# Optimization experiments

Hardware: AMD Instinct MI355X
Metric: run time of the kernel (lower is better)

The kernel has to match this reference:

```python
import jax, jax.numpy as jnp
import numpy as np

K, Q, DIM = 64, 128, 1024
TF_W, DE_W, FFT_W = 1.0, 0.8, 0.6  # opt.TF_weight / DE_weight / FFT_weight


def setup_inputs() -> dict:
    key = jax.random.key(0)
    ks = jax.random.split(key, 9)
    def feats(k):
        return jax.random.normal(k, (K, Q, DIM), dtype=jnp.float32)
    def protos(k):
        return jax.random.normal(k, (K, DIM), dtype=jnp.float32)
    def var(k):
        # positive variances, bounded away from zero
        return jax.random.uniform(k, (K,), dtype=jnp.float32) + 0.5
    return {
        "TFq_output": feats(ks[0]), "TFs_proto": protos(ks[1]), "TF_variance": var(ks[2]),
        "DEq_output": feats(ks[3]), "DEs_proto": protos(ks[4]), "DE_variance": var(ks[5]),
        "FFTq_output": feats(ks[6]), "FFTs_proto": protos(ks[7]), "FFT_variance": var(ks[8]),
    }


def _mah_dist(xq, proto, variance):
    # ||x - p||^2 / var via expansion: avoids materializing (num, protonum, dim)
    x2 = jnp.sum(xq * xq, axis=1, keepdims=True)            # (num, 1)
    p2 = jnp.sum(proto * proto, axis=1)[None, :]            # (1, protonum)
    xp = xq @ proto.T                                       # (num, protonum)
    return (x2 - 2.0 * xp + p2) / variance[None, :]


def _modality(xq, proto, variance, w):
    logits = -_mah_dist(xq, proto, variance)
    pred = w * jax.nn.softmax(logits, axis=1)
    mahloss = -(w * jax.nn.log_softmax(logits, axis=1))
    return pred, mahloss


def reference(TFq_output, TFs_proto, TF_variance,
              DEq_output, DEs_proto, DE_variance,
              FFTq_output, FFTs_proto, FFT_variance):
    k, q, _ = TFq_output.shape
    y = jnp.repeat(jnp.arange(k), q)                         # (k*q,)

    tf_pred, tf_loss = _modality(TFq_output.reshape(k * q, -1), TFs_proto, TF_variance, TF_W)
    de_pred, de_loss = _modality(DEq_output.reshape(k * q, -1), DEs_proto, DE_variance, DE_W)
    fft_pred, fft_loss = _modality(FFTq_output.reshape(k * q, -1), FFTs_proto, FFT_variance, FFT_W)

    fusion_loss = tf_loss + de_loss + fft_loss               # (k*q, k)
    loss = jnp.take_along_axis(fusion_loss, y[:, None], axis=1).squeeze(-1).mean()

    pred_mah = tf_pred + de_pred + fft_pred
    pred = jnp.argmax(pred_mah, axis=1)
    acc = (pred == y).astype(jnp.float32).mean()
    return (loss, acc)
```

## Files before the change

kernel.cpp:

```cpp
#include <hip/hip_runtime.h>


typedef _Float16 half8 __attribute__((ext_vector_type(8)));
typedef float    floatx4 __attribute__((ext_vector_type(4)));

#define NCLS   64
#define QPC    128
#define DIM    1024
#define NROWS  (NCLS * QPC)
#define KSPLIT 4
#define KSLICE (DIM / KSPLIT)
#define NITER  (KSLICE / 32)
#define NWAVES 12
#define DSTRIDE 17
#define PSTRIDE 65

#define WPROTO_BYTES (3 * NCLS * DIM * 2)
#define WS_NEED      (WPROTO_BYTES + 3 * NCLS * 4)

__global__ __launch_bounds__(64) void prep_protos(
    const float* __restrict__ Ptf, const float* __restrict__ Pde,
    const float* __restrict__ Pff, _Float16* __restrict__ W,
    float* __restrict__ p2)
{
    const int m    = blockIdx.x >> 5;
    const int kcg  = blockIdx.x & 31;
    const int lane = threadIdx.x;
    const int l15  = lane & 15;
    const int quad = lane >> 4;
    const float* __restrict__ P = (m == 0) ? Ptf : (m == 1) ? Pde : Pff;

    #pragma unroll
    for (int t = 0; t < 4; ++t) {
        const float* src = P + (size_t)(t * 16 + l15) * DIM + kcg * 32 + quad * 8;
        const float4 b0 = *reinterpret_cast<const float4*>(src);
        const float4 b1 = *reinterpret_cast<const float4*>(src + 4);
        half8 h;
        h[0] = (_Float16)b0.x; h[1] = (_Float16)b0.y;
        h[2] = (_Float16)b0.z; h[3] = (_Float16)b0.w;
        h[4] = (_Float16)b1.x; h[5] = (_Float16)b1.y;
        h[6] = (_Float16)b1.z; h[7] = (_Float16)b1.w;
        *reinterpret_cast<half8*>(W + ((size_t)(m * 32 + kcg) * 4 + t) * 512 + lane * 8) = h;

        float s = b0.x*b0.x + b0.y*b0.y + b0.z*b0.z + b0.w*b0.w
                + b1.x*b1.x + b1.y*b1.y + b1.z*b1.z + b1.w*b1.w;
        s += __shfl_xor(s, 16);
        s += __shfl_xor(s, 32);
        if (quad == 0) atomicAdd(&p2[m * 64 + t * 16 + l15], s);
    }
}

__global__ __launch_bounds__(NWAVES * 64, 3) void fusion_loss_kernel(
    const float* __restrict__ Xtf, const float* __restrict__ Vtf,
    const float* __restrict__ Xde, const float* __restrict__ Vde,
    const float* __restrict__ Xff, const float* __restrict__ Vff,
    const _Float16* __restrict__ W, const float* __restrict__ p2g,
    float* __restrict__ out)
{
    __shared__ float dpart[NWAVES][64 * DSTRIDE];
    __shared__ float x2part[NWAVES][16];
    __shared__ float predL[16 * PSTRIDE];
    __shared__ float lossL;

    const int tid  = threadIdx.x;
    const int wave = tid >> 6;
    const int lane = tid & 63;
    const int l15  = lane & 15;
    const int quad = lane >> 4;
    const int m    = wave >> 2;
    const int kq   = wave & 3;
    const int rowBase = blockIdx.x * 16;

    for (int i = tid; i < 16 * PSTRIDE; i += NWAVES * 64) predL[i] = 0.0f;
    if (tid == 0) lossL = 0.0f;

    const float* __restrict__ X = (m == 0) ? Xtf : (m == 1) ? Xde : Xff;
    const float* __restrict__ V = (m == 0) ? Vtf : (m == 1) ? Vde : Vff;
    const float  w = (m == 0) ? 1.0f : (m == 1) ? 0.8f : 0.6f;

    floatx4 d[4];
    #pragma unroll
    for (int t = 0; t < 4; ++t) d[t] = (floatx4){0.f, 0.f, 0.f, 0.f};
    float x2p = 0.0f;

    const float* xrow = X + (size_t)(rowBase + l15) * DIM + kq * KSLICE + quad * 8;
    const _Float16* wbase = W + (size_t)(m * 32 + kq * NITER) * 4 * 512 + lane * 8;

    #pragma unroll 4
    for (int kc = 0; kc < NITER; ++kc) {
        const int ko = kc * 32;
        const float4 a0 = *reinterpret_cast<const float4*>(xrow + ko);
        const float4 a1 = *reinterpret_cast<const float4*>(xrow + ko + 4);
        half8 bf[4];
        #pragma unroll
        for (int t = 0; t < 4; ++t)
            bf[t] = *reinterpret_cast<const half8*>(wbase + (size_t)(kc * 4 + t) * 512);

        x2p += a0.x*a0.x + a0.y*a0.y + a0.z*a0.z + a0.w*a0.w
             + a1.x*a1.x + a1.y*a1.y + a1.z*a1.z + a1.w*a1.w;

        half8 af;
        af[0] = (_Float16)a0.x; af[1] = (_Float16)a0.y;
        af[2] = (_Float16)a0.z; af[3] = (_Float16)a0.w;
        af[4] = (_Float16)a1.x; af[5] = (_Float16)a1.y;
        af[6] = (_Float16)a1.z; af[7] = (_Float16)a1.w;

        #pragma unroll
        for (int t = 0; t < 4; ++t)
            d[t] = __builtin_amdgcn_mfma_f32_16x16x32_f16(af, bf[t], d[t], 0, 0, 0);
    }

    x2p += __shfl_xor(x2p, 16);
    x2p += __shfl_xor(x2p, 32);

    {
        float* dp = &dpart[wave][lane * DSTRIDE];
        #pragma unroll
        for (int t = 0; t < 4; ++t)
            *reinterpret_cast<float4*>(dp + t * 4) =
                make_float4(d[t][0], d[t][1], d[t][2], d[t][3]);
        if (quad == 0) x2part[wave][l15] = x2p;
    }
    __syncthreads();

    const int y = rowBase >> 7;

    if (kq == 0) {
        floatx4 dsum[4];
        #pragma unroll
        for (int t = 0; t < 4; ++t) dsum[t] = (floatx4){0.f, 0.f, 0.f, 0.f};
        float x2r[4] = {0.f, 0.f, 0.f, 0.f};
        #pragma unroll
        for (int k2 = 0; k2 < KSPLIT; ++k2) {
            const int wv = m * 4 + k2;
            const float* src = &dpart[wv][lane * DSTRIDE];
            #pragma unroll
            for (int t = 0; t < 4; ++t) {
                const float4 v = *reinterpret_cast<const float4*>(src + t * 4);
                dsum[t][0] += v.x; dsum[t][1] += v.y; dsum[t][2] += v.z; dsum[t][3] += v.w;
            }
            #pragma unroll
            for (int r = 0; r < 4; ++r) x2r[r] += x2part[wv][quad * 4 + r];
        }
        float vc[4], p2c[4];
        #pragma unroll
        for (int t = 0; t < 4; ++t) {
            vc[t]  = V[t * 16 + l15];
            p2c[t] = p2g[m * 64 + t * 16 + l15];
        }

        float lossAcc = 0.0f;
        #pragma unroll
        for (int r = 0; r < 4; ++r) {
            float lg[4];
            #pragma unroll
            for (int t = 0; t < 4; ++t)
                lg[t] = (2.0f * dsum[t][r] - x2r[r] - p2c[t]) / vc[t];

            float mx = fmaxf(fmaxf(lg[0], lg[1]), fmaxf(lg[2], lg[3]));
            #pragma unroll
            for (int dl = 1; dl <= 8; dl <<= 1) mx = fmaxf(mx, __shfl_xor(mx, dl));
            float s = expf(lg[0] - mx) + expf(lg[1] - mx)
                    + expf(lg[2] - mx) + expf(lg[3] - mx);
            #pragma unroll
            for (int dl = 1; dl <= 8; dl <<= 1) s += __shfl_xor(s, dl);
            const float lse = mx + logf(s);

            const int row = quad * 4 + r;
            #pragma unroll
            for (int t = 0; t < 4; ++t) {
                const int col = t * 16 + l15;
                if (col == y) lossAcc += w * (lse - lg[t]);
                atomicAdd(&predL[row * PSTRIDE + col], w * expf(lg[t] - lse));
            }
        }
        #pragma unroll
        for (int dl = 1; dl <= 32; dl <<= 1) lossAcc += __shfl_xor(lossAcc, dl);
        if (lane == 0) atomicAdd(&lossL, lossAcc);
    }
    __syncthreads();

    if (wave == 0) {
        float cnt = 0.0f;
        #pragma unroll 1
        for (int r = 0; r < 16; ++r) {
            float bv = predL[r * PSTRIDE + lane];
            int   bc = lane;
            #pragma unroll
            for (int dl = 1; dl <= 32; dl <<= 1) {
                const float ov = __shfl_xor(bv, dl);
                const int   oc = __shfl_xor(bc, dl);
                if (ov > bv || (ov == bv && oc < bc)) { bv = ov; bc = oc; }
            }
            if (lane == 0 && bc == y) cnt += 1.0f;
        }
        if (lane == 0) {
            atomicAdd(&out[0], lossL * (1.0f / NROWS));
            atomicAdd(&out[1], cnt * (1.0f / NROWS));
        }
    }
}

__global__ __launch_bounds__(NWAVES * 64) void fusion_loss_fallback(
    const float* __restrict__ Xtf, const float* __restrict__ Ptf, const float* __restrict__ Vtf,
    const float* __restrict__ Xde, const float* __restrict__ Pde, const float* __restrict__ Vde,
    const float* __restrict__ Xff, const float* __restrict__ Pff, const float* __restrict__ Vff,
    float* __restrict__ out)
{
    __shared__ float dpart[NWAVES][64 * DSTRIDE];
    __shared__ float x2part[NWAVES][16];
    __shared__ float p2part[NWAVES][64];
    __shared__ float predL[16 * PSTRIDE];
    __shared__ float lossL;

    const int tid  = threadIdx.x;
    const int wave = tid >> 6;
    const int lane = tid & 63;
    const int l15  = lane & 15;
    const int quad = lane >> 4;
    const int m    = wave >> 2;
    const int kq   = wave & 3;
    const int rowBase = blockIdx.x * 16;

    for (int i = tid; i < 16 * PSTRIDE; i += NWAVES * 64) predL[i] = 0.0f;
    if (tid == 0) lossL = 0.0f;

    const float* __restrict__ X = (m == 0) ? Xtf : (m == 1) ? Xde : Xff;
    const float* __restrict__ P = (m == 0) ? Ptf : (m == 1) ? Pde : Pff;
    const float* __restrict__ V = (m == 0) ? Vtf : (m == 1) ? Vde : Vff;
    const float  w = (m == 0) ? 1.0f : (m == 1) ? 0.8f : 0.6f;

    floatx4 d[4];
    #pragma unroll
    for (int t = 0; t < 4; ++t) d[t] = (floatx4){0.f, 0.f, 0.f, 0.f};
    float x2p    = 0.0f;
    float p2p[4] = {0.f, 0.f, 0.f, 0.f};

    const float* xrow = X + (size_t)(rowBase + l15) * DIM + kq * KSLICE + quad * 8;
    const float* prow[4];
    #pragma unroll
    for (int t = 0; t < 4; ++t)
        prow[t] = P + (size_t)(t * 16 + l15) * DIM + kq * KSLICE + quad * 8;

    #pragma unroll 2
    for (int kc = 0; kc < NITER; ++kc) {
        const int ko = kc * 32;
        const float4 a0 = *reinterpret_cast<const float4*>(xrow + ko);
        const float4 a1 = *reinterpret_cast<const float4*>(xrow + ko + 4);
        float4 b0[4], b1[4];
        #pragma unroll
        for (int t = 0; t < 4; ++t) {
            b0[t] = *reinterpret_cast<const float4*>(prow[t] + ko);
            b1[t] = *reinterpret_cast<const float4*>(prow[t] + ko + 4);
        }
        x2p += a0.x*a0.x + a0.y*a0.y + a0.z*a0.z + a0.w*a0.w
             + a1.x*a1.x + a1.y*a1.y + a1.z*a1.z + a1.w*a1.w;
        half8 af;
        af[0] = (_Float16)a0.x; af[1] = (_Float16)a0.y;
        af[2] = (_Float16)a0.z; af[3] = (_Float16)a0.w;
        af[4] = (_Float16)a1.x; af[5] = (_Float16)a1.y;
        af[6] = (_Float16)a1.z; af[7] = (_Float16)a1.w;
        #pragma unroll
        for (int t = 0; t < 4; ++t) {
            p2p[t] += b0[t].x*b0[t].x + b0[t].y*b0[t].y + b0[t].z*b0[t].z + b0[t].w*b0[t].w
                    + b1[t].x*b1[t].x + b1[t].y*b1[t].y + b1[t].z*b1[t].z + b1[t].w*b1[t].w;
            half8 bf;
            bf[0] = (_Float16)b0[t].x; bf[1] = (_Float16)b0[t].y;
            bf[2] = (_Float16)b0[t].z; bf[3] = (_Float16)b0[t].w;
            bf[4] = (_Float16)b1[t].x; bf[5] = (_Float16)b1[t].y;
            bf[6] = (_Float16)b1[t].z; bf[7] = (_Float16)b1[t].w;
            d[t] = __builtin_amdgcn_mfma_f32_16x16x32_f16(af, bf, d[t], 0, 0, 0);
        }
    }

    x2p += __shfl_xor(x2p, 16);
    x2p += __shfl_xor(x2p, 32);
    #pragma unroll
    for (int t = 0; t < 4; ++t) {
        p2p[t] += __shfl_xor(p2p[t], 16);
        p2p[t] += __shfl_xor(p2p[t], 32);
    }
    {
        float* dp = &dpart[wave][lane * DSTRIDE];
        #pragma unroll
        for (int t = 0; t < 4; ++t)
            *reinterpret_cast<float4*>(dp + t * 4) =
                make_float4(d[t][0], d[t][1], d[t][2], d[t][3]);
        if (quad == 0) {
            x2part[wave][l15] = x2p;
            #pragma unroll
            for (int t = 0; t < 4; ++t) p2part[wave][t * 16 + l15] = p2p[t];
        }
    }
    __syncthreads();

    const int y = rowBase >> 7;

    if (kq == 0) {
        floatx4 dsum[4];
        #pragma unroll
        for (int t = 0; t < 4; ++t) dsum[t] = (floatx4){0.f, 0.f, 0.f, 0.f};
        float x2r[4] = {0.f, 0.f, 0.f, 0.f};
        float p2c[4] = {0.f, 0.f, 0.f, 0.f};
        #pragma unroll
        for (int k2 = 0; k2 < KSPLIT; ++k2) {
            const int wv = m * 4 + k2;
            const float* src = &dpart[wv][lane * DSTRIDE];
            #pragma unroll
            for (int t = 0; t < 4; ++t) {
                const float4 v = *reinterpret_cast<const float4*>(src + t * 4);
                dsum[t][0] += v.x; dsum[t][1] += v.y; dsum[t][2] += v.z; dsum[t][3] += v.w;
            }
            #pragma unroll
            for (int r = 0; r < 4; ++r) x2r[r] += x2part[wv][quad * 4 + r];
            #pragma unroll
            for (int t = 0; t < 4; ++t) p2c[t] += p2part[wv][t * 16 + l15];
        }
        float vc[4];
        #pragma unroll
        for (int t = 0; t < 4; ++t) vc[t] = V[t * 16 + l15];

        float lossAcc = 0.0f;
        #pragma unroll
        for (int r = 0; r < 4; ++r) {
            float lg[4];
            #pragma unroll
            for (int t = 0; t < 4; ++t)
                lg[t] = (2.0f * dsum[t][r] - x2r[r] - p2c[t]) / vc[t];
            float mx = fmaxf(fmaxf(lg[0], lg[1]), fmaxf(lg[2], lg[3]));
            #pragma unroll
            for (int dl = 1; dl <= 8; dl <<= 1) mx = fmaxf(mx, __shfl_xor(mx, dl));
            float s = expf(lg[0] - mx) + expf(lg[1] - mx)
                    + expf(lg[2] - mx) + expf(lg[3] - mx);
            #pragma unroll
            for (int dl = 1; dl <= 8; dl <<= 1) s += __shfl_xor(s, dl);
            const float lse = mx + logf(s);
            const int row = quad * 4 + r;
            #pragma unroll
            for (int t = 0; t < 4; ++t) {
                const int col = t * 16 + l15;
                if (col == y) lossAcc += w * (lse - lg[t]);
                atomicAdd(&predL[row * PSTRIDE + col], w * expf(lg[t] - lse));
            }
        }
        #pragma unroll
        for (int dl = 1; dl <= 32; dl <<= 1) lossAcc += __shfl_xor(lossAcc, dl);
        if (lane == 0) atomicAdd(&lossL, lossAcc);
    }
    __syncthreads();

    if (wave == 0) {
        float cnt = 0.0f;
        #pragma unroll 1
        for (int r = 0; r < 16; ++r) {
            float bv = predL[r * PSTRIDE + lane];
            int   bc = lane;
            #pragma unroll
            for (int dl = 1; dl <= 32; dl <<= 1) {
                const float ov = __shfl_xor(bv, dl);
                const int   oc = __shfl_xor(bc, dl);
                if (ov > bv || (ov == bv && oc < bc)) { bv = ov; bc = oc; }
            }
            if (lane == 0 && bc == y) cnt += 1.0f;
        }
        if (lane == 0) {
            atomicAdd(&out[0], lossL * (1.0f / NROWS));
            atomicAdd(&out[1], cnt * (1.0f / NROWS));
        }
    }
}

extern "C" void kernel_launch(void* const* d_in, const int* in_sizes, int n_in,
                              void* d_out, int out_size, void* d_ws, size_t ws_size,
                              hipStream_t stream) {
    const float* Xtf = (const float*)d_in[0];
    const float* Ptf = (const float*)d_in[1];
    const float* Vtf = (const float*)d_in[2];
    const float* Xde = (const float*)d_in[3];
    const float* Pde = (const float*)d_in[4];
    const float* Vde = (const float*)d_in[5];
    const float* Xff = (const float*)d_in[6];
    const float* Pff = (const float*)d_in[7];
    const float* Vff = (const float*)d_in[8];
    float* out = (float*)d_out;

    hipMemsetAsync(out, 0, 2 * sizeof(float), stream);

    if (ws_size >= (size_t)WS_NEED) {
        _Float16* W  = (_Float16*)d_ws;
        float*    p2 = (float*)((char*)d_ws + WPROTO_BYTES);
        hipMemsetAsync(p2, 0, 3 * NCLS * sizeof(float), stream);
        prep_protos<<<dim3(96), dim3(64), 0, stream>>>(Ptf, Pde, Pff, W, p2);
        fusion_loss_kernel<<<dim3(NROWS / 16), dim3(NWAVES * 64), 0, stream>>>(
            Xtf, Vtf, Xde, Vde, Xff, Vff, W, p2, out);
    } else {
        fusion_loss_fallback<<<dim3(NROWS / 16), dim3(NWAVES * 64), 0, stream>>>(
            Xtf, Ptf, Vtf, Xde, Pde, Vde, Xff, Pff, Vff, out);
    }
}
```

Baseline: 170.3 us.

## Split modalities across blocks, stage X via LDS DMA, finalize with separate kernels

```diff
diff --git a/kernel.cpp b/kernel.cpp
--- a/kernel.cpp
+++ b/kernel.cpp
@@ -8,15 +8,27 @@
 #define QPC    128
 #define DIM    1024
 #define NROWS  (NCLS * QPC)
-#define KSPLIT 4
-#define KSLICE (DIM / KSPLIT)
-#define NITER  (KSLICE / 32)
-#define NWAVES 12
-#define DSTRIDE 17
-#define PSTRIDE 65
-
-#define WPROTO_BYTES (3 * NCLS * DIM * 2)
-#define WS_NEED      (WPROTO_BYTES + 3 * NCLS * 4)
+#define NRT    (NROWS / 16)
+#define CHUNK  256
+#define NCHUNK (DIM / CHUNK)
+#define NKC    (CHUNK / 32)
+#define UW     264
+
+#define OFF_W    0
+#define W_BYTES  (3 * NCLS * DIM * 2)
+#define OFF_P2   W_BYTES
+#define OFF_PRED 397312
+#define PRED_BYTES (3 * NROWS * NCLS * 4)
+#define OFF_LOSS (OFF_PRED + PRED_BYTES)
+#define OFF_CNT  (OFF_LOSS + 1536 * 4)
+#define WS_NEED  (OFF_CNT + 64 * 4)
+
+__device__ __forceinline__ void dma16(const float* g, float* l) {
+    __builtin_amdgcn_global_load_lds(
+        (const __attribute__((address_space(1))) void*)g,
+        (__attribute__((address_space(3))) void*)l,
+        16, 0, 0);
+}
 
 __global__ __launch_bounds__(64) void prep_protos(
     const float* __restrict__ Ptf, const float* __restrict__ Pde,
@@ -50,156 +62,197 @@
     }
 }
 
-__global__ __launch_bounds__(NWAVES * 64, 3) void fusion_loss_kernel(
+__global__ __launch_bounds__(128) void fusion_main(
     const float* __restrict__ Xtf, const float* __restrict__ Vtf,
     const float* __restrict__ Xde, const float* __restrict__ Vde,
     const float* __restrict__ Xff, const float* __restrict__ Vff,
     const _Float16* __restrict__ W, const float* __restrict__ p2g,
-    float* __restrict__ out)
+    float* __restrict__ predOut,
+    float* __restrict__ lossPart)
 {
-    __shared__ float dpart[NWAVES][64 * DSTRIDE];
-    __shared__ float x2part[NWAVES][16];
-    __shared__ float predL[16 * PSTRIDE];
-    __shared__ float lossL;
+    __shared__ float chunkBuf[16 * UW];
+    __shared__ float mxW[2][16], sW[2][16];
+    __shared__ float lossW[2];
 
     const int tid  = threadIdx.x;
-    const int wave = tid >> 6;
+    const int w    = tid >> 6;
     const int lane = tid & 63;
     const int l15  = lane & 15;
     const int quad = lane >> 4;
-    const int m    = wave >> 2;
-    const int kq   = wave & 3;
-    const int rowBase = blockIdx.x * 16;
-
-    for (int i = tid; i < 16 * PSTRIDE; i += NWAVES * 64) predL[i] = 0.0f;
-    if (tid == 0) lossL = 0.0f;
+    const int m    = blockIdx.x >> 9;
+    const int rt   = blockIdx.x & 511;
+    const int rowBase = rt * 16;
 
     const float* __restrict__ X = (m == 0) ? Xtf : (m == 1) ? Xde : Xff;
     const float* __restrict__ V = (m == 0) ? Vtf : (m == 1) ? Vde : Vff;
-    const float  w = (m == 0) ? 1.0f : (m == 1) ? 0.8f : 0.6f;
-
-    floatx4 d[4];
-    #pragma unroll
-    for (int t = 0; t < 4; ++t) d[t] = (floatx4){0.f, 0.f, 0.f, 0.f};
+    const float  wgt = (m == 0) ? 1.0f : (m == 1) ? 0.8f : 0.6f;
+
+    floatx4 d[2];
+    d[0] = (floatx4){0.f, 0.f, 0.f, 0.f};
+    d[1] = (floatx4){0.f, 0.f, 0.f, 0.f};
     float x2p = 0.0f;
 
-    const float* xrow = X + (size_t)(rowBase + l15) * DIM + kq * KSLICE + quad * 8;
-    const _Float16* wbase = W + (size_t)(m * 32 + kq * NITER) * 4 * 512 + lane * 8;
-
-    #pragma unroll 4
-    for (int kc = 0; kc < NITER; ++kc) {
-        const int ko = kc * 32;
-        const float4 a0 = *reinterpret_cast<const float4*>(xrow + ko);
-        const float4 a1 = *reinterpret_cast<const float4*>(xrow + ko + 4);
-        half8 bf[4];
-        #pragma unroll
-        for (int t = 0; t < 4; ++t)
-            bf[t] = *reinterpret_cast<const half8*>(wbase + (size_t)(kc * 4 + t) * 512);
-
-        x2p += a0.x*a0.x + a0.y*a0.y + a0.z*a0.z + a0.w*a0.w
-             + a1.x*a1.x + a1.y*a1.y + a1.z*a1.z + a1.w*a1.w;
-
-        half8 af;
-        af[0] = (_Float16)a0.x; af[1] = (_Float16)a0.y;
-        af[2] = (_Float16)a0.z; af[3] = (_Float16)a0.w;
-        af[4] = (_Float16)a1.x; af[5] = (_Float16)a1.y;
-        af[6] = (_Float16)a1.z; af[7] = (_Float16)a1.w;
-
-        #pragma unroll
-        for (int t = 0; t < 4; ++t)
-            d[t] = __builtin_amdgcn_mfma_f32_16x16x32_f16(af, bf[t], d[t], 0, 0, 0);
+    #pragma unroll 1
+    for (int c = 0; c < NCHUNK; ++c) {
+        __syncthreads();
+        const float* gbase = X + (size_t)rowBase * DIM + c * CHUNK + lane * 4;
+        #pragma unroll
+        for (int r8 = 0; r8 < 8; ++r8) {
+            const int r = w * 8 + r8;
+            dma16(gbase + (size_t)r * DIM, &chunkBuf[r * UW]);
+        }
+        __syncthreads();
+
+        #pragma unroll
+        for (int kc = 0; kc < NKC; ++kc) {
+            const int off = l15 * UW + kc * 32 + quad * 8;
+            const float4 a0 = *reinterpret_cast<const float4*>(&chunkBuf[off]);
+            const float4 a1 = *reinterpret_cast<const float4*>(&chunkBuf[off + 4]);
+
+            const int kcg = c * NKC + kc;
+            half8 bf[2];
+            #pragma unroll
+            for (int t = 0; t < 2; ++t)
+                bf[t] = *reinterpret_cast<const half8*>(
+                    W + ((size_t)(m * 32 + kcg) * 4 + (w * 2 + t)) * 512 + lane * 8);
+
+            x2p += a0.x*a0.x + a0.y*a0.y + a0.z*a0.z + a0.w*a0.w
+                 + a1.x*a1.x + a1.y*a1.y + a1.z*a1.z + a1.w*a1.w;
+
+            half8 af;
+            af[0] = (_Float16)a0.x; af[1] = (_Float16)a0.y;
+            af[2] = (_Float16)a0.z; af[3] = (_Float16)a0.w;
+            af[4] = (_Float16)a1.x; af[5] = (_Float16)a1.y;
+            af[6] = (_Float16)a1.z; af[7] = (_Float16)a1.w;
+
+            d[0] = __builtin_amdgcn_mfma_f32_16x16x32_f16(af, bf[0], d[0], 0, 0, 0);
+            d[1] = __builtin_amdgcn_mfma_f32_16x16x32_f16(af, bf[1], d[1], 0, 0, 0);
+        }
     }
 
     x2p += __shfl_xor(x2p, 16);
     x2p += __shfl_xor(x2p, 32);
-
-    {
-        float* dp = &dpart[wave][lane * DSTRIDE];
-        #pragma unroll
-        for (int t = 0; t < 4; ++t)
-            *reinterpret_cast<float4*>(dp + t * 4) =
-                make_float4(d[t][0], d[t][1], d[t][2], d[t][3]);
-        if (quad == 0) x2part[wave][l15] = x2p;
+    float x2r[4];
+    #pragma unroll
+    for (int r = 0; r < 4; ++r) x2r[r] = __shfl(x2p, quad * 4 + r);
+
+    float vc[2], p2c[2];
+    #pragma unroll
+    for (int t = 0; t < 2; ++t) {
+        const int col = w * 32 + t * 16 + l15;
+        vc[t]  = V[col];
+        p2c[t] = p2g[m * 64 + col];
+    }
+
+    float lg[4][2];
+    #pragma unroll
+    for (int r = 0; r < 4; ++r)
+        #pragma unroll
+        for (int t = 0; t < 2; ++t)
+            lg[r][t] = (2.0f * d[t][r] - x2r[r] - p2c[t]) / vc[t];
+
+    #pragma unroll
+    for (int r = 0; r < 4; ++r) {
+        float mx = fmaxf(lg[r][0], lg[r][1]);
+        #pragma unroll
+        for (int dl = 1; dl <= 8; dl <<= 1) mx = fmaxf(mx, __shfl_xor(mx, dl));
+        if (l15 == 0) mxW[w][quad * 4 + r] = mx;
+    }
+    __syncthreads();
+    float gmx[4];
+    #pragma unroll
+    for (int r = 0; r < 4; ++r) {
+        const int row = quad * 4 + r;
+        gmx[r] = fmaxf(mxW[0][row], mxW[1][row]);
+        float s = expf(lg[r][0] - gmx[r]) + expf(lg[r][1] - gmx[r]);
+        #pragma unroll
+        for (int dl = 1; dl <= 8; dl <<= 1) s += __shfl_xor(s, dl);
+        if (l15 == 0) sW[w][row] = s;
     }
     __syncthreads();
 
     const int y = rowBase >> 7;
-
-    if (kq == 0) {
-        floatx4 dsum[4];
-        #pragma unroll
-        for (int t = 0; t < 4; ++t) dsum[t] = (floatx4){0.f, 0.f, 0.f, 0.f};
-        float x2r[4] = {0.f, 0.f, 0.f, 0.f};
-        #pragma unroll
-        for (int k2 = 0; k2 < KSPLIT; ++k2) {
-            const int wv = m * 4 + k2;
-            const float* src = &dpart[wv][lane * DSTRIDE];
-            #pragma unroll
-            for (int t = 0; t < 4; ++t) {
-                const float4 v = *reinterpret_cast<const float4*>(src + t * 4);
-                dsum[t][0] += v.x; dsum[t][1] += v.y; dsum[t][2] += v.z; dsum[t][3] += v.w;
-            }
-            #pragma unroll
-            for (int r = 0; r < 4; ++r) x2r[r] += x2part[wv][quad * 4 + r];
-        }
-        float vc[4], p2c[4];
-        #pragma unroll
-        for (int t = 0; t < 4; ++t) {
-            vc[t]  = V[t * 16 + l15];
-            p2c[t] = p2g[m * 64 + t * 16 + l15];
-        }
-
-        float lossAcc = 0.0f;
-        #pragma unroll
-        for (int r = 0; r < 4; ++r) {
-            float lg[4];
-            #pragma unroll
-            for (int t = 0; t < 4; ++t)
-                lg[t] = (2.0f * dsum[t][r] - x2r[r] - p2c[t]) / vc[t];
-
-            float mx = fmaxf(fmaxf(lg[0], lg[1]), fmaxf(lg[2], lg[3]));
-            #pragma unroll
-            for (int dl = 1; dl <= 8; dl <<= 1) mx = fmaxf(mx, __shfl_xor(mx, dl));
-            float s = expf(lg[0] - mx) + expf(lg[1] - mx)
-                    + expf(lg[2] - mx) + expf(lg[3] - mx);
-            #pragma unroll
-            for (int dl = 1; dl <= 8; dl <<= 1) s += __shfl_xor(s, dl);
-            const float lse = mx + logf(s);
-
-            const int row = quad * 4 + r;
-            #pragma unroll
-            for (int t = 0; t < 4; ++t) {
-                const int col = t * 16 + l15;
-                if (col == y) lossAcc += w * (lse - lg[t]);
-                atomicAdd(&predL[row * PSTRIDE + col], w * expf(lg[t] - lse));
-            }
-        }
-        #pragma unroll
-        for (int dl = 1; dl <= 32; dl <<= 1) lossAcc += __shfl_xor(lossAcc, dl);
-        if (lane == 0) atomicAdd(&lossL, lossAcc);
-    }
-    __syncthreads();
-
-    if (wave == 0) {
-        float cnt = 0.0f;
-        #pragma unroll 1
-        for (int r = 0; r < 16; ++r) {
-            float bv = predL[r * PSTRIDE + lane];
-            int   bc = lane;
-            #pragma unroll
-            for (int dl = 1; dl <= 32; dl <<= 1) {
-                const float ov = __shfl_xor(bv, dl);
-                const int   oc = __shfl_xor(bc, dl);
-                if (ov > bv || (ov == bv && oc < bc)) { bv = ov; bc = oc; }
-            }
-            if (lane == 0 && bc == y) cnt += 1.0f;
-        }
-        if (lane == 0) {
-            atomicAdd(&out[0], lossL * (1.0f / NROWS));
-            atomicAdd(&out[1], cnt * (1.0f / NROWS));
-        }
-    }
-}
+    float lossAcc = 0.0f;
+    #pragma unroll
+    for (int r = 0; r < 4; ++r) {
+        const int row = quad * 4 + r;
+        const float lse = gmx[r] + logf(sW[0][row] + sW[1][row]);
+        if (w == (y >> 5) && l15 == (y & 15))
+            lossAcc += wgt * (lse - lg[r][(y >> 4) & 1]);
+        const int R = rowBase + row;
+        #pragma unroll
+        for (int t = 0; t < 2; ++t)
+            predOut[((size_t)m * NROWS + R) * 64 + w * 32 + t * 16 + l15] =
+                wgt * expf(lg[r][t] - lse);
+    }
+
+    #pragma unroll
+    for (int dl = 1; dl <= 32; dl <<= 1) lossAcc += __shfl_xor(lossAcc, dl);
+    if (lane == 0) lossW[w] = lossAcc;
+    __syncthreads();
+    if (tid == 0) lossPart[blockIdx.x] = lossW[0] + lossW[1];
+}
+
+__global__ __launch_bounds__(256) void finalize1(
+    const float* __restrict__ pred, float* __restrict__ cntPart)
+{
+    const int tid  = threadIdx.x;
+    const int w    = tid >> 6;
+    const int lane = tid & 63;
+    float cnt = 0.0f;
+    #pragma unroll 1
+    for (int i = 0; i < 32; ++i) {
+        const int R = blockIdx.x * 128 + w * 32 + i;
+        float p = pred[(size_t)R * 64 + lane]
+                + pred[((size_t)NROWS + R) * 64 + lane]
+                + pred[((size_t)2 * NROWS + R) * 64 + lane];
+        float bv = p; int bc = lane;
+        #pragma unroll
+        for (int dl = 1; dl <= 32; dl <<= 1) {
+            const float ov = __shfl_xor(bv, dl);
+            const int   oc = __shfl_xor(bc, dl);
+            if (ov > bv || (ov == bv && oc < bc)) { bv = ov; bc = oc; }
+        }
+        if (lane == 0 && bc == (R >> 7)) cnt += 1.0f;
+    }
+    #pragma unroll
+    for (int dl = 1; dl <= 32; dl <<= 1) cnt += __shfl_xor(cnt, dl);
+    __shared__ float sc[4];
+    if (lane == 0) sc[w] = cnt;
+    __syncthreads();
+    if (tid == 0) cntPart[blockIdx.x] = sc[0] + sc[1] + sc[2] + sc[3];
+}
+
+__global__ __launch_bounds__(256) void finalize2(
+    const float* __restrict__ lossPart, const float* __restrict__ cntPart,
+    float* __restrict__ out)
+{
+    const int tid  = threadIdx.x;
+    const int lane = tid & 63;
+    const int w    = tid >> 6;
+    float l = 0.0f, c = 0.0f;
+    for (int i = tid; i < 1536; i += 256) l += lossPart[i];
+    if (tid < 64) c = cntPart[tid];
+    #pragma unroll
+    for (int dl = 1; dl <= 32; dl <<= 1) {
+        l += __shfl_xor(l, dl);
+        c += __shfl_xor(c, dl);
+    }
+    __shared__ float sl[4], sc[4];
+    if (lane == 0) { sl[w] = l; sc[w] = c; }
+    __syncthreads();
+    if (tid == 0) {
+        out[0] = (sl[0] + sl[1] + sl[2] + sl[3]) * (1.0f / NROWS);
+        out[1] = (sc[0] + sc[1] + sc[2] + sc[3]) * (1.0f / NROWS);
+    }
+}
+
+#define NWAVES 12
+#define KSPLIT 4
+#define KSLICE (DIM / KSPLIT)
+#define NITER  (KSLICE / 32)
+#define DSTRIDE 17
+#define PSTRIDE 65
 
 __global__ __launch_bounds__(NWAVES * 64) void fusion_loss_fallback(
     const float* __restrict__ Xtf, const float* __restrict__ Ptf, const float* __restrict__ Vtf,
@@ -384,16 +437,22 @@
     const float* Vff = (const float*)d_in[8];
     float* out = (float*)d_out;
 
-    hipMemsetAsync(out, 0, 2 * sizeof(float), stream);
-
     if (ws_size >= (size_t)WS_NEED) {
-        _Float16* W  = (_Float16*)d_ws;
-        float*    p2 = (float*)((char*)d_ws + WPROTO_BYTES);
+        char* ws = (char*)d_ws;
+        _Float16* W    = (_Float16*)(ws + OFF_W);
+        float*    p2   = (float*)(ws + OFF_P2);
+        float*    pred = (float*)(ws + OFF_PRED);
+        float*    lossP= (float*)(ws + OFF_LOSS);
+        float*    cntP = (float*)(ws + OFF_CNT);
+
         hipMemsetAsync(p2, 0, 3 * NCLS * sizeof(float), stream);
         prep_protos<<<dim3(96), dim3(64), 0, stream>>>(Ptf, Pde, Pff, W, p2);
-        fusion_loss_kernel<<<dim3(NROWS / 16), dim3(NWAVES * 64), 0, stream>>>(
-            Xtf, Vtf, Xde, Vde, Xff, Vff, W, p2, out);
+        fusion_main<<<dim3(3 * NRT), dim3(128), 0, stream>>>(
+            Xtf, Vtf, Xde, Vde, Xff, Vff, W, p2, pred, lossP);
+        finalize1<<<dim3(NROWS / 128), dim3(256), 0, stream>>>(pred, cntP);
+        finalize2<<<dim3(1), dim3(256), 0, stream>>>(lossP, cntP, out);
     } else {
+        hipMemsetAsync(out, 0, 2 * sizeof(float), stream);
         fusion_loss_fallback<<<dim3(NROWS / 16), dim3(NWAVES * 64), 0, stream>>>(
             Xtf, Ptf, Vtf, Xde, Pde, Vde, Xff, Pff, Vff, out);
     }
```

Result: slower. 175.5 us (+3.0%).
